# Performance work log

Measured on AMD Instinct MI355X. Metric: run time of the kernel, lower is better.

Reference implementation:

```python
import jax, jax.numpy as jnp
import numpy as np

# ---- static configuration (matches init_kwargs / input_specs) ----
B, DIM, H, W = 2, 32, 512, 512
FOLD, P, HDIM, NCLS, CV = 8, 2, 96, 16, 96
S = P * P                      # superpixels per tile
h, w = H // FOLD, W // FOLD    # 64, 64 tile size
N = h * w                      # pixels per tile

# ---- static SSN neighbor tables (init label map -> 9 candidate spixels) ----
_lab = np.repeat(np.repeat(np.arange(S).reshape(P, P), h // P, 0), w // P, 1).reshape(-1)
_sy, _sx = _lab // P, _lab % P
_dy = np.repeat(np.array([-1, 0, 1]), 3)[:, None]
_dx = np.tile(np.array([-1, 0, 1]), 3)[:, None]
_ny, _nx = _sy[None] + _dy, _sx[None] + _dx
_valid = (_ny >= 0) & (_ny < P) & (_nx >= 0) & (_nx < P)
NBR = jnp.asarray(np.where(_valid, _ny * P + _nx, 0), dtype=jnp.int32)  # [9,N]
VALID = jnp.asarray(_valid)                                             # [9,N]

def _conv1x1(x, Wk, bk):
    return jnp.einsum('oc,bchw->bohw', Wk, x) + bk[None, :, None, None]

def _tiles(t):  # 'b c (f1 h) (f2 w) -> (b f1 f2) c h w'
    Bq, C = t.shape[:2]
    return t.reshape(Bq, C, FOLD, h, FOLD, w).transpose(0, 2, 4, 1, 3, 5).reshape(Bq * FOLD * FOLD, C, h, w)

def _pool(t):  # adaptive avg pool (h,w)->(P,P); returns [b,C,S]
    b, C = t.shape[:2]
    return t.reshape(b, C, P, h // P, P, w // P).mean((3, 5)).reshape(b, C, S)

def _affinity(Fp, cen):
    # Fp [b,Ctot,N], cen [b,Ctot,S]; squared-euclid dist pixel->9 neighbor spixels,
    # sparse softmax over the 9 candidates, then scatter to dense [b,S,N] affinity.
    d = (Fp * Fp).sum(1)[:, None, :] + (cen * cen).sum(1)[:, :, None] \
        - 2.0 * jnp.einsum('bcn,bcs->bsn', Fp, cen)          # [b,S,N]
    b = Fp.shape[0]
    idx = jnp.broadcast_to(NBR[None], (b, 9, N))
    d9 = jnp.where(VALID[None], jnp.take_along_axis(d, idx, axis=1), 1e16)
    aff = jax.nn.softmax(-d9, axis=1)                        # [b,9,N]
    bi = jnp.arange(b)[:, None, None]
    ni = jnp.arange(N)[None, None, :]
    return jnp.zeros((b, S, N), Fp.dtype).at[bi, idx, ni].add(jnp.where(VALID[None], aff, 0.0))

def setup_inputs():
    k = jax.random.split(jax.random.key(0), 6)
    return {
        'x': jax.random.normal(k[0], (B, DIM, H, W), jnp.float32),
        'feat': jax.random.normal(k[1], (B, CV, H, W), jnp.float32),
        'sdf_data': jax.random.normal(k[2], (B, DIM - 1, H, W), jnp.float32),
        'Wf': 0.1 * jax.random.normal(k[3], (HDIM, DIM), jnp.float32),
        'bf': jnp.zeros((HDIM,), jnp.float32),
        'Wsdf': 0.1 * jax.random.normal(k[4], (HDIM, DIM - 1), jnp.float32),
        'bsdf': jnp.zeros((HDIM,), jnp.float32),
        'gt': jax.random.randint(k[5], (B, H, W), 0, NCLS, jnp.int32),
    }

def _cluster(x, feat, sdf_data, Wf, bf, Wsdf, bsdf):
    hsi = _conv1x1(x, Wf, bf)
    sdf = _conv1x1(sdf_data, Wsdf, bsdf)
    pf = _tiles(feat).reshape(-1, CV, N)      # per-tile pixel (value) features
    df = _tiles(hsi).reshape(-1, HDIM, N)     # deep features
    sf = _tiles(sdf).reshape(-1, HDIM, N)     # sdf features
    b = pf.shape[0]
    cen_pf = _pool(pf.reshape(b, CV, h, w))
    cen_df = _pool(df.reshape(b, HDIM, h, w))
    cen_sf = _pool(sf.reshape(b, HDIM, h, w))
    value_centers = cen_pf.transpose(0, 2, 1)                # [b,S,C]
    Fall = jnp.concatenate([pf, df, sf], 1)
    # SSN iter 0: soft affinity, update pixel-feature centroids
    A0 = _affinity(Fall, jnp.concatenate([cen_pf, cen_df, cen_sf], 1))
    cen_pf = jnp.einsum('bsn,bcn->bcs', A0, pf) / (A0.sum(-1)[:, None, :] + 1e-16)
    # SSN iter 1 (last): final dense affinity; torch computes this under no_grad
    sim = jax.lax.stop_gradient(_affinity(Fall, jnp.concatenate([cen_pf, cen_df, cen_sf], 1)))
    mask = jax.nn.one_hot(jnp.argmax(sim, 1), S, axis=1, dtype=sim.dtype)   # hard argmax mask [b,S,N]
    sim = sim * mask
    out = (jnp.einsum('bsn,bnc->bsc', sim, pf.transpose(0, 2, 1)) + value_centers) \
          / (sim.sum(-1, keepdims=True) + 1.0)
    center_feat = out.reshape(B, FOLD * FOLD * S, CV)
    mask5 = mask.reshape(B, FOLD * FOLD, S, h, w)
    return center_feat, mask5

def _gen_labels(gt, mask5):
    T = FOLD * FOLD
    coef = jnp.arange(S, dtype=mask5.dtype).reshape(1, 1, S, 1, 1)
    small = (mask5 * coef).sum(2) + jnp.arange(0, T * S, S, dtype=mask5.dtype).reshape(1, T, 1, 1)
    spix_map = small.reshape(B, FOLD, FOLD, h, w).transpose(0, 1, 3, 2, 4).reshape(B, H, W)
    gt_r = gt.reshape(B, FOLD, h, FOLD, w).transpose(0, 1, 3, 2, 4).reshape(B, T, h, w) + 1
    gt_filt = (gt_r[:, :, None].astype(mask5.dtype) * mask5).reshape(B, T, S, N).astype(jnp.int32)
    count = jax.nn.one_hot(gt_filt, NCLS + 1, dtype=jnp.float32).sum(3)   # [B,T,S,NCLS+1]
    labels = count[..., 1:].transpose(0, 3, 1, 2).reshape(B, NCLS, T * S)
    return labels, spix_map

def reference(x, feat, sdf_data, Wf, bf, Wsdf, bsdf, gt):
    center_feat, mask5 = _cluster(x, feat, sdf_data, Wf, bf, Wsdf, bsdf)
    labels, spix_map = _gen_labels(gt, jax.lax.stop_gradient(mask5))
    return center_feat, labels, spix_map
```

## Files before the change

### kernel.cpp

```cpp
#include <hip/hip_runtime.h>
#include <hip/hip_bf16.h>


#define OFF_POOLX   0
#define OFF_POOLS   16384
#define OFF_CENPF0  32256
#define OFF_UDF     81408
#define OFF_USF     97792
#define OFF_GCONST  113664
#define OFF_NORM0   114176
#define OFF_NUM1    114688
#define OFF_DEN1    163840
#define OFF_CENPF1  164352
#define OFF_NORM1   213504
#define OFF_OUTNUM  214016
#define OFF_OUTDEN  263168
#define OFF_LABELS  263680
#define OFF_G       271872
#define ZERO_BASE   OFF_NUM1
#define ZERO_LEN    157184

#define OUT_CF 0
#define OUT_LB 49152
#define OUT_SP 57344

typedef float f32x4 __attribute__((ext_vector_type(4)));
typedef short bf16x8 __attribute__((ext_vector_type(8)));
typedef unsigned short u16x4 __attribute__((ext_vector_type(4)));

__device__ __forceinline__ float bf2f(unsigned short u) {
  return __uint_as_float(((unsigned)u) << 16);
}
__device__ __forceinline__ unsigned short f2bf(float f) {
  return (unsigned short)(__float_as_uint(f) >> 16);
}

__global__ __launch_bounds__(256) void k_pool(const float* __restrict__ x,
    const float* __restrict__ feat, const float* __restrict__ sdf,
    float* __restrict__ ws) {
  int plane = blockIdx.x, f1 = blockIdx.y, tid = threadIdx.x;
  {
    int lb = blockIdx.y * gridDim.x + blockIdx.x;
    if (tid < 64) {
      int zi = lb * 64 + tid;
      if (zi < ZERO_LEN) ws[ZERO_BASE + zi] = 0.f;
    }
  }
  int b = plane / 159, ch = plane % 159;
  const float* src; int c, C, cls;
  if (ch < 32)      { src = x;    C = 32; c = ch;      cls = 0; }
  else if (ch < 63) { src = sdf;  C = 31; c = ch - 32; cls = 1; }
  else              { src = feat; C = 96; c = ch - 63; cls = 2; }
  const float* base = src + ((size_t)(b*C + c)*512 + f1*64)*512;
  int half = tid >> 7, col4 = tid & 127;
  const float* p0 = base + (size_t)half*512 + (size_t)col4*4;
  f32x4 v[16];
  float acc0 = 0.f, acc1 = 0.f;
  #pragma unroll
  for (int i = 0; i < 16; ++i)
    v[i] = *reinterpret_cast<const f32x4*>(p0 + (size_t)i*1024);
  #pragma unroll
  for (int i = 0; i < 16; ++i) { f32x4 t = v[i]; acc0 += t[0] + t[1] + t[2] + t[3]; }
  #pragma unroll
  for (int i = 0; i < 16; ++i)
    v[i] = *reinterpret_cast<const f32x4*>(p0 + (size_t)(16 + i)*1024);
  #pragma unroll
  for (int i = 0; i < 16; ++i) { f32x4 t = v[i]; acc1 += t[0] + t[1] + t[2] + t[3]; }
  acc0 += __shfl_xor(acc0, 1, 64); acc0 += __shfl_xor(acc0, 2, 64); acc0 += __shfl_xor(acc0, 4, 64);
  acc1 += __shfl_xor(acc1, 1, 64); acc1 += __shfl_xor(acc1, 2, 64); acc1 += __shfl_xor(acc1, 4, 64);
  __shared__ float part[32][2];
  int lane = tid & 63;
  if ((lane & 7) == 0) {
    int f2 = col4 >> 4, qx = (col4 >> 3) & 1;
    part[(f2*2 + qx)*2 + 0][half] = acc0;
    part[(f2*2 + qx)*2 + 1][half] = acc1;
  }
  __syncthreads();
  if (tid < 32) {
    float v2 = (part[tid][0] + part[tid][1]) * (1.f/1024.f);
    int f2 = tid >> 2, qx = (tid >> 1) & 1, qy = tid & 1;
    int tile = b*64 + f1*8 + f2, s = qy*2 + qx;
    float* dst;
    if (cls == 0)      dst = ws + OFF_POOLX  + (tile*32 + c)*4;
    else if (cls == 1) dst = ws + OFF_POOLS  + (tile*31 + c)*4;
    else               dst = ws + OFF_CENPF0 + (tile*96 + c)*4;
    dst[s] = v2;
  }
}

__global__ __launch_bounds__(384) void k_centers(const float* __restrict__ Wf,
    const float* __restrict__ bfv, const float* __restrict__ Wsdf,
    const float* __restrict__ bsdf, float* __restrict__ ws) {
  int tile = blockIdx.x, tid = threadIdx.x;
  __shared__ float px[128];
  __shared__ float ps[124];
  __shared__ float cdf[384];
  __shared__ float csf[384];
  __shared__ float redg[4], redn[4];
  if (tid < 128) px[tid] = ws[OFF_POOLX + tile*128 + tid];
  if (tid < 124) ps[tid] = ws[OFF_POOLS + tile*124 + tid];
  if (tid < 4) { redg[tid] = 0.f; redn[tid] = 0.f; }
  __syncthreads();
  int c = tid % 96, s = tid / 96;
  float bc = bfv[c];
  float a = bc;
  for (int k = 0; k < 32; ++k) a += Wf[c*32 + k] * px[k*4 + s];
  cdf[c*4 + s] = a;
  float bs = bsdf[c];
  float a2 = bs;
  for (int k = 0; k < 31; ++k) a2 += Wsdf[c*31 + k] * ps[k*4 + s];
  csf[c*4 + s] = a2;
  atomicAdd(&redg[s], 2.f*(bc*a + bs*a2) - (a*a + a2*a2));
  float cp = ws[OFF_CENPF0 + tile*384 + c*4 + s];
  atomicAdd(&redn[s], cp*cp);
  __syncthreads();
  if (tid < 128) {
    int s2 = tid >> 5, k = tid & 31;
    float u = 0.f;
    for (int c2 = 0; c2 < 96; ++c2) u += Wf[c2*32 + k] * cdf[c2*4 + s2];
    ws[OFF_UDF + tile*128 + tid] = u;
  } else if (tid < 252) {
    int t2 = tid - 128, s2 = t2 / 31, k = t2 % 31;
    float u = 0.f;
    for (int c2 = 0; c2 < 96; ++c2) u += Wsdf[c2*31 + k] * csf[c2*4 + s2];
    ws[OFF_USF + tile*124 + t2] = u;
  }
  if (tid < 4) { ws[OFF_GCONST + tile*4 + tid] = redg[tid]; ws[OFF_NORM0 + tile*4 + tid] = redn[tid]; }
}

__global__ __launch_bounds__(256) void k_pass2(const float* __restrict__ x,
    const float* __restrict__ feat, const float* __restrict__ sdf,
    float* __restrict__ ws) {
  int wg = blockIdx.x, tile = wg >> 2, seg = wg & 3, tid = threadIdx.x;
  int b = tile >> 6, tl = tile & 63, f1 = tl >> 3, f2 = tl & 7;
  __shared__ float s_cpf0[384];
  __shared__ float s_udf[128];
  __shared__ float s_usf[124];
  __shared__ float s_gc[4], s_n0[4];
  __shared__ __align__(16) unsigned short s_pfT[96][264];
  __shared__ __align__(16) unsigned short s_aT[16][264];
  __shared__ __align__(16) float s_part[2][8][260];
  for (int i = tid; i < 384; i += 256) s_cpf0[i] = ws[OFF_CENPF0 + tile*384 + i];
  if (tid < 128) s_udf[tid] = ws[OFF_UDF + tile*128 + tid];
  if (tid < 124) s_usf[tid] = ws[OFF_USF + tile*124 + tid];
  if (tid < 4) { s_gc[tid] = ws[OFF_GCONST + tile*4 + tid]; s_n0[tid] = ws[OFF_NORM0 + tile*4 + tid]; }
  for (int i = tid; i < 16*264; i += 256) (&s_aT[0][0])[i] = 0;
  __syncthreads();
  int lane = tid & 63, wave = tid >> 6;
  int mrow = lane & 15, quad = lane >> 4;
  int q4 = lane * 4;
  f32x4 zero4 = {0.f, 0.f, 0.f, 0.f};
  f32x4 accC[6] = {zero4, zero4, zero4, zero4, zero4, zero4};
  float dden[4] = {0.f, 0.f, 0.f, 0.f};
  for (int chunk = 0; chunk < 4; ++chunk) {
    int pq = seg*1024 + chunk*256 + q4;
    int goq = (f1*64 + (pq >> 6))*512 + f2*64 + (pq & 63);
    const float* xq = x   + (size_t)(b*32)*262144 + goq;
    const float* sq = sdf + (size_t)(b*31)*262144 + goq;
    const float* fq = feat+ (size_t)(b*96)*262144 + goq;
    f32x4 dpd[4] = {zero4, zero4, zero4, zero4};
    f32x4 dpp[4] = {zero4, zero4, zero4, zero4};
    f32x4 vv[8];
    #pragma unroll
    for (int i = 0; i < 8; ++i)
      vv[i] = *reinterpret_cast<const f32x4*>(xq + (size_t)(wave + 4*i)*262144);
    #pragma unroll
    for (int i = 0; i < 8; ++i) {
      int ch = wave + 4*i;
      #pragma unroll
      for (int s = 0; s < 4; ++s) dpd[s] += vv[i] * s_udf[s*32 + ch];
    }
    #pragma unroll
    for (int i = 0; i < 8; ++i)
      if (wave + 4*i < 31)
        vv[i] = *reinterpret_cast<const f32x4*>(sq + (size_t)(wave + 4*i)*262144);
    #pragma unroll
    for (int i = 0; i < 8; ++i) {
      int ch = wave + 4*i;
      if (ch < 31) {
        #pragma unroll
        for (int s = 0; s < 4; ++s) dpd[s] += vv[i] * s_usf[s*31 + ch];
      }
    }
    #pragma unroll
    for (int r = 0; r < 3; ++r) {
      #pragma unroll
      for (int i = 0; i < 8; ++i)
        vv[i] = *reinterpret_cast<const f32x4*>(fq + (size_t)(wave + 4*(r*8 + i))*262144);
      #pragma unroll
      for (int i = 0; i < 8; ++i) {
        int ch = wave + 4*(r*8 + i);
        u16x4 uu = { f2bf(vv[i][0]), f2bf(vv[i][1]), f2bf(vv[i][2]), f2bf(vv[i][3]) };
        *reinterpret_cast<u16x4*>(&s_pfT[ch][q4]) = uu;
        #pragma unroll
        for (int s = 0; s < 4; ++s) dpp[s] += vv[i] * s_cpf0[ch*4 + s];
      }
    }
    if (wave >= 2) {
      #pragma unroll
      for (int s = 0; s < 4; ++s) {
        *reinterpret_cast<f32x4*>(&s_part[wave-2][s][q4]) = dpd[s];
        *reinterpret_cast<f32x4*>(&s_part[wave-2][4+s][q4]) = dpp[s];
      }
    }
    __syncthreads();
    if (wave < 2) {
      #pragma unroll
      for (int s = 0; s < 4; ++s) {
        f32x4 t = *reinterpret_cast<f32x4*>(&s_part[wave][s][q4]);
        t += dpd[s];
        *reinterpret_cast<f32x4*>(&s_part[wave][s][q4]) = t;
        f32x4 t2 = *reinterpret_cast<f32x4*>(&s_part[wave][4+s][q4]);
        t2 += dpp[s];
        *reinterpret_cast<f32x4*>(&s_part[wave][4+s][q4]) = t2;
      }
    }
    __syncthreads();
    float d0 = s_part[0][0][tid] + s_part[1][0][tid];
    float d1 = s_part[0][1][tid] + s_part[1][1][tid];
    float d2 = s_part[0][2][tid] + s_part[1][2][tid];
    float d3 = s_part[0][3][tid] + s_part[1][3][tid];
    float p0 = s_part[0][4][tid] + s_part[1][4][tid];
    float p1 = s_part[0][5][tid] + s_part[1][5][tid];
    float p2 = s_part[0][6][tid] + s_part[1][6][tid];
    float p3 = s_part[0][7][tid] + s_part[1][7][tid];
    float g0 = 2.f*d0 + s_gc[0], g1 = 2.f*d1 + s_gc[1];
    float g2 = 2.f*d2 + s_gc[2], g3 = 2.f*d3 + s_gc[3];
    int p = seg*1024 + chunk*256 + tid;
    {
      f32x4 gv = {g0, g1, g2, g3};
      *reinterpret_cast<f32x4*>(ws + OFF_G + ((size_t)tile << 14) + (size_t)p*4) = gv;
    }
    float sc0 = g0 + 2.f*p0 - s_n0[0];
    float sc1 = g1 + 2.f*p1 - s_n0[1];
    float sc2 = g2 + 2.f*p2 - s_n0[2];
    float sc3 = g3 + 2.f*p3 - s_n0[3];
    float m = fmaxf(fmaxf(sc0, sc1), fmaxf(sc2, sc3));
    float e0 = expf(sc0 - m), e1 = expf(sc1 - m), e2 = expf(sc2 - m), e3 = expf(sc3 - m);
    float inv = 1.f / (e0 + e1 + e2 + e3);
    float a0 = e0*inv, a1 = e1*inv, a2 = e2*inv, a3 = e3*inv;
    s_aT[0][tid] = f2bf(a0); s_aT[1][tid] = f2bf(a1);
    s_aT[2][tid] = f2bf(a2); s_aT[3][tid] = f2bf(a3);
    dden[0] += a0; dden[1] += a1; dden[2] += a2; dden[3] += a3;
    __syncthreads();
    #pragma unroll
    for (int kk = 0; kk < 2; ++kk) {
      int k0 = (wave*2 + kk)*32 + quad*8;
      bf16x8 bfrag = *reinterpret_cast<const bf16x8*>(&s_aT[mrow][k0]);
      #pragma unroll
      for (int mt = 0; mt < 6; ++mt) {
        bf16x8 afrag = *reinterpret_cast<const bf16x8*>(&s_pfT[mt*16 + mrow][k0]);
        accC[mt] = __builtin_amdgcn_mfma_f32_16x16x32_bf16(afrag, bfrag, accC[mt], 0, 0, 0);
      }
    }
    __syncthreads();
  }
  if (mrow < 4) {
    #pragma unroll
    for (int mt = 0; mt < 6; ++mt)
      #pragma unroll
      for (int r = 0; r < 4; ++r) {
        int c = mt*16 + quad*4 + r;
        atomicAdd(&ws[OFF_NUM1 + (tile*96 + c)*4 + mrow], accC[mt][r]);
      }
  }
  for (int m2 = 1; m2 < 64; m2 <<= 1) {
    dden[0] += __shfl_xor(dden[0], m2, 64); dden[1] += __shfl_xor(dden[1], m2, 64);
    dden[2] += __shfl_xor(dden[2], m2, 64); dden[3] += __shfl_xor(dden[3], m2, 64);
  }
  if (lane == 0) {
    atomicAdd(&ws[OFF_DEN1 + tile*4 + 0], dden[0]);
    atomicAdd(&ws[OFF_DEN1 + tile*4 + 1], dden[1]);
    atomicAdd(&ws[OFF_DEN1 + tile*4 + 2], dden[2]);
    atomicAdd(&ws[OFF_DEN1 + tile*4 + 3], dden[3]);
  }
}

__global__ __launch_bounds__(256) void k_pass3(const float* __restrict__ feat,
    const int* __restrict__ gt, float* __restrict__ ws, float* __restrict__ out) {
  int wg = blockIdx.x, tile = wg >> 2, seg = wg & 3, tid = threadIdx.x;
  int b = tile >> 6, tl = tile & 63, f1 = tl >> 3, f2 = tl & 7;
  __shared__ float s_cpf1[384];
  __shared__ float s_n1[4];
  __shared__ __align__(16) unsigned short s_pfT[96][264];
  __shared__ __align__(16) unsigned short s_aT[16][264];
  __shared__ __align__(16) float s_part[2][4][260];
  __shared__ float s_hist[64];
  if (tid < 4) s_n1[tid] = 0.f;
  if (tid < 64) s_hist[tid] = 0.f;
  for (int i = tid; i < 16*264; i += 256) (&s_aT[0][0])[i] = 0;
  __syncthreads();
  for (int i = tid; i < 384; i += 256) {
    float den = ws[OFF_DEN1 + tile*4 + (i & 3)];
    float v = ws[OFF_NUM1 + tile*384 + i] / (den + 1e-16f);
    s_cpf1[i] = v;
    atomicAdd(&s_n1[i & 3], v*v);
  }
  __syncthreads();
  int lane = tid & 63, wave = tid >> 6;
  int mrow = lane & 15, quad = lane >> 4;
  int q4 = lane * 4;
  f32x4 zero4 = {0.f, 0.f, 0.f, 0.f};
  f32x4 accC[6] = {zero4, zero4, zero4, zero4, zero4, zero4};
  float oden[4] = {0.f, 0.f, 0.f, 0.f};
  for (int chunk = 0; chunk < 4; ++chunk) {
    int pq = seg*1024 + chunk*256 + q4;
    int goq = (f1*64 + (pq >> 6))*512 + f2*64 + (pq & 63);
    const float* fq = feat + (size_t)(b*96)*262144 + goq;
    f32x4 dpp[4] = {zero4, zero4, zero4, zero4};
    f32x4 vv[8];
    #pragma unroll
    for (int r = 0; r < 3; ++r) {
      #pragma unroll
      for (int i = 0; i < 8; ++i)
        vv[i] = *reinterpret_cast<const f32x4*>(fq + (size_t)(wave + 4*(r*8 + i))*262144);
      #pragma unroll
      for (int i = 0; i < 8; ++i) {
        int ch = wave + 4*(r*8 + i);
        u16x4 uu = { f2bf(vv[i][0]), f2bf(vv[i][1]), f2bf(vv[i][2]), f2bf(vv[i][3]) };
        *reinterpret_cast<u16x4*>(&s_pfT[ch][q4]) = uu;
        #pragma unroll
        for (int s = 0; s < 4; ++s) dpp[s] += vv[i] * s_cpf1[ch*4 + s];
      }
    }
    if (wave >= 2) {
      #pragma unroll
      for (int s = 0; s < 4; ++s)
        *reinterpret_cast<f32x4*>(&s_part[wave-2][s][q4]) = dpp[s];
    }
    __syncthreads();
    if (wave < 2) {
      #pragma unroll
      for (int s = 0; s < 4; ++s) {
        f32x4 t = *reinterpret_cast<f32x4*>(&s_part[wave][s][q4]);
        t += dpp[s];
        *reinterpret_cast<f32x4*>(&s_part[wave][s][q4]) = t;
      }
    }
    __syncthreads();
    int p = seg*1024 + chunk*256 + tid;
    int y = p >> 6, xx = p & 63;
    int go = (f1*64 + y)*512 + f2*64 + xx;
    f32x4 gv = *reinterpret_cast<const f32x4*>(ws + OFF_G + ((size_t)tile << 14) + (size_t)p*4);
    float p0 = s_part[0][0][tid] + s_part[1][0][tid];
    float p1 = s_part[0][1][tid] + s_part[1][1][tid];
    float p2 = s_part[0][2][tid] + s_part[1][2][tid];
    float p3 = s_part[0][3][tid] + s_part[1][3][tid];
    float sc0 = gv[0] + 2.f*p0 - s_n1[0];
    float sc1 = gv[1] + 2.f*p1 - s_n1[1];
    float sc2 = gv[2] + 2.f*p2 - s_n1[2];
    float sc3 = gv[3] + 2.f*p3 - s_n1[3];
    int ss = 0; float best = sc0;
    if (sc1 > best) { best = sc1; ss = 1; }
    if (sc2 > best) { best = sc2; ss = 2; }
    if (sc3 > best) { best = sc3; ss = 3; }
    float se = expf(sc0-best) + expf(sc1-best) + expf(sc2-best) + expf(sc3-best);
    float sim = 1.f / se;
    unsigned short sb = f2bf(sim);
    s_aT[0][tid] = (ss == 0) ? sb : (unsigned short)0;
    s_aT[1][tid] = (ss == 1) ? sb : (unsigned short)0;
    s_aT[2][tid] = (ss == 2) ? sb : (unsigned short)0;
    s_aT[3][tid] = (ss == 3) ? sb : (unsigned short)0;
    oden[ss] += sim;
    int gvv = gt[b*262144 + go];
    atomicAdd(&s_hist[ss*16 + gvv], 1.f);
    out[OUT_SP + b*262144 + go] = (float)(tl*4 + ss);
    __syncthreads();
    #pragma unroll
    for (int kk = 0; kk < 2; ++kk) {
      int k0 = (wave*2 + kk)*32 + quad*8;
      bf16x8 bfrag = *reinterpret_cast<const bf16x8*>(&s_aT[mrow][k0]);
      #pragma unroll
      for (int mt = 0; mt < 6; ++mt) {
        bf16x8 afrag = *reinterpret_cast<const bf16x8*>(&s_pfT[mt*16 + mrow][k0]);
        accC[mt] = __builtin_amdgcn_mfma_f32_16x16x32_bf16(afrag, bfrag, accC[mt], 0, 0, 0);
      }
    }
    __syncthreads();
  }
  if (mrow < 4) {
    #pragma unroll
    for (int mt = 0; mt < 6; ++mt)
      #pragma unroll
      for (int r = 0; r < 4; ++r) {
        int c = mt*16 + quad*4 + r;
        atomicAdd(&ws[OFF_OUTNUM + (tile*96 + c)*4 + mrow], accC[mt][r]);
      }
  }
  for (int m2 = 1; m2 < 64; m2 <<= 1) {
    oden[0] += __shfl_xor(oden[0], m2, 64); oden[1] += __shfl_xor(oden[1], m2, 64);
    oden[2] += __shfl_xor(oden[2], m2, 64); oden[3] += __shfl_xor(oden[3], m2, 64);
  }
  if (lane == 0) {
    atomicAdd(&ws[OFF_OUTDEN + tile*4 + 0], oden[0]);
    atomicAdd(&ws[OFF_OUTDEN + tile*4 + 1], oden[1]);
    atomicAdd(&ws[OFF_OUTDEN + tile*4 + 2], oden[2]);
    atomicAdd(&ws[OFF_OUTDEN + tile*4 + 3], oden[3]);
  }
  if (tid < 64) atomicAdd(&ws[OFF_LABELS + tile*64 + tid], s_hist[tid]);
}

__global__ __launch_bounds__(384) void k_out(const float* __restrict__ ws,
                                             float* __restrict__ out) {
  int tile = blockIdx.x, tid = threadIdx.x;
  int b = tile >> 6, tl = tile & 63;
  int c = tid % 96, s = tid / 96;
  float od = ws[OFF_OUTDEN + tile*4 + s];
  float v = (ws[OFF_OUTNUM + (tile*96 + c)*4 + s] + ws[OFF_CENPF0 + (tile*96 + c)*4 + s]) / (od + 1.f);
  out[OUT_CF + (size_t)(b*256 + tl*4 + s)*96 + c] = v;
  if (tid < 64) {
    int s2 = tid >> 4, cls = tid & 15;
    float cnt = ws[OFF_LABELS + tile*64 + tid];
    out[OUT_LB + (b*16 + cls)*256 + tl*4 + s2] = cnt;
  }
}

extern "C" void kernel_launch(void* const* d_in, const int* in_sizes, int n_in,
                              void* d_out, int out_size, void* d_ws, size_t ws_size,
                              hipStream_t stream) {
  const float* x    = (const float*)d_in[0];
  const float* feat = (const float*)d_in[1];
  const float* sdf  = (const float*)d_in[2];
  const float* Wf   = (const float*)d_in[3];
  const float* bfv  = (const float*)d_in[4];
  const float* Wsdf = (const float*)d_in[5];
  const float* bsdf = (const float*)d_in[6];
  const int* gt = (const int*)d_in[7];
  float* ws = (float*)d_ws;
  float* out = (float*)d_out;

  k_pool   <<<dim3(318, 8), 256, 0, stream>>>(x, feat, sdf, ws);
  k_centers<<<128, 384, 0, stream>>>(Wf, bfv, Wsdf, bsdf, ws);
  k_pass2  <<<512, 256, 0, stream>>>(x, feat, sdf, ws);
  k_pass3  <<<512, 256, 0, stream>>>(feat, gt, ws, out);
  k_out    <<<128, 384, 0, stream>>>(ws, out);
}
```

Measured before the change: 491.8 us.

## Fuse center computation into pass2 and prefetch next chunk loads in registers

Removes the k_centers launch and recomputes the per-tile center projections inside k_pass2, four times redundantly per tile, using the s_pfT buffer as scratch. Both pass kernels now software-pipeline the global loads. The next chunk's x/sdf/feat (and G/gt in pass3) go into registers while the current chunk is being computed. Launch bounds are set to 2 waves/SIMD. The register-held prefetch (~40 f32x4) raises register pressure and may spill, and the redundant center compute adds serial work before the main loop.

```diff
diff --git a/kernel.cpp b/kernel.cpp
--- a/kernel.cpp
+++ b/kernel.cpp
@@ -5,14 +5,8 @@
 #define OFF_POOLX   0
 #define OFF_POOLS   16384
 #define OFF_CENPF0  32256
-#define OFF_UDF     81408
-#define OFF_USF     97792
-#define OFF_GCONST  113664
-#define OFF_NORM0   114176
 #define OFF_NUM1    114688
 #define OFF_DEN1    163840
-#define OFF_CENPF1  164352
-#define OFF_NORM1   213504
 #define OFF_OUTNUM  214016
 #define OFF_OUTDEN  263168
 #define OFF_LABELS  263680
@@ -24,13 +18,12 @@
 #define OUT_LB 49152
 #define OUT_SP 57344
 
+#define PL 262144
+
 typedef float f32x4 __attribute__((ext_vector_type(4)));
 typedef short bf16x8 __attribute__((ext_vector_type(8)));
 typedef unsigned short u16x4 __attribute__((ext_vector_type(4)));
 
-__device__ __forceinline__ float bf2f(unsigned short u) {
-  return __uint_as_float(((unsigned)u) << 16);
-}
 __device__ __forceinline__ unsigned short f2bf(float f) {
   return (unsigned short)(__float_as_uint(f) >> 16);
 }
@@ -88,48 +81,10 @@
   }
 }
 
-__global__ __launch_bounds__(384) void k_centers(const float* __restrict__ Wf,
-    const float* __restrict__ bfv, const float* __restrict__ Wsdf,
-    const float* __restrict__ bsdf, float* __restrict__ ws) {
-  int tile = blockIdx.x, tid = threadIdx.x;
-  __shared__ float px[128];
-  __shared__ float ps[124];
-  __shared__ float cdf[384];
-  __shared__ float csf[384];
-  __shared__ float redg[4], redn[4];
-  if (tid < 128) px[tid] = ws[OFF_POOLX + tile*128 + tid];
-  if (tid < 124) ps[tid] = ws[OFF_POOLS + tile*124 + tid];
-  if (tid < 4) { redg[tid] = 0.f; redn[tid] = 0.f; }
-  __syncthreads();
-  int c = tid % 96, s = tid / 96;
-  float bc = bfv[c];
-  float a = bc;
-  for (int k = 0; k < 32; ++k) a += Wf[c*32 + k] * px[k*4 + s];
-  cdf[c*4 + s] = a;
-  float bs = bsdf[c];
-  float a2 = bs;
-  for (int k = 0; k < 31; ++k) a2 += Wsdf[c*31 + k] * ps[k*4 + s];
-  csf[c*4 + s] = a2;
-  atomicAdd(&redg[s], 2.f*(bc*a + bs*a2) - (a*a + a2*a2));
-  float cp = ws[OFF_CENPF0 + tile*384 + c*4 + s];
-  atomicAdd(&redn[s], cp*cp);
-  __syncthreads();
-  if (tid < 128) {
-    int s2 = tid >> 5, k = tid & 31;
-    float u = 0.f;
-    for (int c2 = 0; c2 < 96; ++c2) u += Wf[c2*32 + k] * cdf[c2*4 + s2];
-    ws[OFF_UDF + tile*128 + tid] = u;
-  } else if (tid < 252) {
-    int t2 = tid - 128, s2 = t2 / 31, k = t2 % 31;
-    float u = 0.f;
-    for (int c2 = 0; c2 < 96; ++c2) u += Wsdf[c2*31 + k] * csf[c2*4 + s2];
-    ws[OFF_USF + tile*124 + t2] = u;
-  }
-  if (tid < 4) { ws[OFF_GCONST + tile*4 + tid] = redg[tid]; ws[OFF_NORM0 + tile*4 + tid] = redn[tid]; }
-}
-
-__global__ __launch_bounds__(256) void k_pass2(const float* __restrict__ x,
+__global__ __launch_bounds__(256, 2) void k_pass2(const float* __restrict__ x,
     const float* __restrict__ feat, const float* __restrict__ sdf,
+    const float* __restrict__ Wf, const float* __restrict__ bfv,
+    const float* __restrict__ Wsdf, const float* __restrict__ bsdf,
     float* __restrict__ ws) {
   int wg = blockIdx.x, tile = wg >> 2, seg = wg & 3, tid = threadIdx.x;
   int b = tile >> 6, tl = tile & 63, f1 = tl >> 3, f2 = tl & 7;
@@ -140,10 +95,46 @@
   __shared__ __align__(16) unsigned short s_pfT[96][264];
   __shared__ __align__(16) unsigned short s_aT[16][264];
   __shared__ __align__(16) float s_part[2][8][260];
+  float* scr  = reinterpret_cast<float*>(&s_pfT[0][0]);
+  float* c_px = scr;
+  float* c_ps = scr + 128;
+  float* c_df = scr + 256;
+  float* c_sf = scr + 640;
   for (int i = tid; i < 384; i += 256) s_cpf0[i] = ws[OFF_CENPF0 + tile*384 + i];
-  if (tid < 128) s_udf[tid] = ws[OFF_UDF + tile*128 + tid];
-  if (tid < 124) s_usf[tid] = ws[OFF_USF + tile*124 + tid];
-  if (tid < 4) { s_gc[tid] = ws[OFF_GCONST + tile*4 + tid]; s_n0[tid] = ws[OFF_NORM0 + tile*4 + tid]; }
+  if (tid < 128) c_px[tid] = ws[OFF_POOLX + tile*128 + tid];
+  if (tid < 124) c_ps[tid] = ws[OFF_POOLS + tile*124 + tid];
+  __syncthreads();
+  for (int i = tid; i < 384; i += 256) {
+    int c = i % 96, s = i / 96;
+    float a = bfv[c];
+    for (int k = 0; k < 32; ++k) a += Wf[c*32 + k] * c_px[k*4 + s];
+    c_df[c*4 + s] = a;
+    float a2 = bsdf[c];
+    for (int k = 0; k < 31; ++k) a2 += Wsdf[c*31 + k] * c_ps[k*4 + s];
+    c_sf[c*4 + s] = a2;
+  }
+  __syncthreads();
+  if (tid < 128) {
+    int s2 = tid >> 5, k = tid & 31;
+    float u = 0.f;
+    for (int c2 = 0; c2 < 96; ++c2) u += Wf[c2*32 + k] * c_df[c2*4 + s2];
+    s_udf[tid] = u;
+  } else if (tid < 252) {
+    int t2 = tid - 128, s2 = t2 / 31, k = t2 % 31;
+    float u = 0.f;
+    for (int c2 = 0; c2 < 96; ++c2) u += Wsdf[c2*31 + k] * c_sf[c2*4 + s2];
+    s_usf[t2] = u;
+  } else {
+    int s = tid - 252;
+    float g = 0.f, n = 0.f;
+    for (int c = 0; c < 96; ++c) {
+      float a = c_df[c*4 + s], a2 = c_sf[c*4 + s];
+      g += 2.f*(bfv[c]*a + bsdf[c]*a2) - (a*a + a2*a2);
+      float cp = s_cpf0[c*4 + s];
+      n += cp*cp;
+    }
+    s_gc[s] = g; s_n0[s] = n;
+  }
   for (int i = tid; i < 16*264; i += 256) (&s_aT[0][0])[i] = 0;
   __syncthreads();
   int lane = tid & 63, wave = tid >> 6;
@@ -152,49 +143,66 @@
   f32x4 zero4 = {0.f, 0.f, 0.f, 0.f};
   f32x4 accC[6] = {zero4, zero4, zero4, zero4, zero4, zero4};
   float dden[4] = {0.f, 0.f, 0.f, 0.f};
+  const float* xb = x   + (size_t)(b*32)*PL;
+  const float* sb = sdf + (size_t)(b*31)*PL;
+  const float* fb = feat+ (size_t)(b*96)*PL;
+  f32x4 xv[8], sv[8], fv[24];
+  {
+    int pq = seg*1024 + q4;
+    int goq = (f1*64 + (pq >> 6))*512 + f2*64 + (pq & 63);
+    #pragma unroll
+    for (int i = 0; i < 8; ++i)
+      xv[i] = *reinterpret_cast<const f32x4*>(xb + (size_t)(wave + 4*i)*PL + goq);
+    #pragma unroll
+    for (int i = 0; i < 8; ++i)
+      if (wave + 4*i < 31)
+        sv[i] = *reinterpret_cast<const f32x4*>(sb + (size_t)(wave + 4*i)*PL + goq);
+    #pragma unroll
+    for (int i = 0; i < 24; ++i)
+      fv[i] = *reinterpret_cast<const f32x4*>(fb + (size_t)(wave + 4*i)*PL + goq);
+  }
   for (int chunk = 0; chunk < 4; ++chunk) {
-    int pq = seg*1024 + chunk*256 + q4;
-    int goq = (f1*64 + (pq >> 6))*512 + f2*64 + (pq & 63);
-    const float* xq = x   + (size_t)(b*32)*262144 + goq;
-    const float* sq = sdf + (size_t)(b*31)*262144 + goq;
-    const float* fq = feat+ (size_t)(b*96)*262144 + goq;
+    int pq1 = seg*1024 + (chunk+1)*256 + q4;
+    int goq1 = (f1*64 + (pq1 >> 6))*512 + f2*64 + (pq1 & 63);
     f32x4 dpd[4] = {zero4, zero4, zero4, zero4};
     f32x4 dpp[4] = {zero4, zero4, zero4, zero4};
-    f32x4 vv[8];
-    #pragma unroll
-    for (int i = 0; i < 8; ++i)
-      vv[i] = *reinterpret_cast<const f32x4*>(xq + (size_t)(wave + 4*i)*262144);
     #pragma unroll
     for (int i = 0; i < 8; ++i) {
       int ch = wave + 4*i;
       #pragma unroll
-      for (int s = 0; s < 4; ++s) dpd[s] += vv[i] * s_udf[s*32 + ch];
-    }
-    #pragma unroll
-    for (int i = 0; i < 8; ++i)
-      if (wave + 4*i < 31)
-        vv[i] = *reinterpret_cast<const f32x4*>(sq + (size_t)(wave + 4*i)*262144);
+      for (int s = 0; s < 4; ++s) dpd[s] += xv[i] * s_udf[s*32 + ch];
+    }
+    if (chunk < 3) {
+      #pragma unroll
+      for (int i = 0; i < 8; ++i)
+        xv[i] = *reinterpret_cast<const f32x4*>(xb + (size_t)(wave + 4*i)*PL + goq1);
+    }
     #pragma unroll
     for (int i = 0; i < 8; ++i) {
       int ch = wave + 4*i;
       if (ch < 31) {
         #pragma unroll
-        for (int s = 0; s < 4; ++s) dpd[s] += vv[i] * s_usf[s*31 + ch];
-      }
-    }
-    #pragma unroll
-    for (int r = 0; r < 3; ++r) {
+        for (int s = 0; s < 4; ++s) dpd[s] += sv[i] * s_usf[s*31 + ch];
+      }
+    }
+    if (chunk < 3) {
       #pragma unroll
       for (int i = 0; i < 8; ++i)
-        vv[i] = *reinterpret_cast<const f32x4*>(fq + (size_t)(wave + 4*(r*8 + i))*262144);
-      #pragma unroll
-      for (int i = 0; i < 8; ++i) {
-        int ch = wave + 4*(r*8 + i);
-        u16x4 uu = { f2bf(vv[i][0]), f2bf(vv[i][1]), f2bf(vv[i][2]), f2bf(vv[i][3]) };
-        *reinterpret_cast<u16x4*>(&s_pfT[ch][q4]) = uu;
-        #pragma unroll
-        for (int s = 0; s < 4; ++s) dpp[s] += vv[i] * s_cpf0[ch*4 + s];
-      }
+        if (wave + 4*i < 31)
+          sv[i] = *reinterpret_cast<const f32x4*>(sb + (size_t)(wave + 4*i)*PL + goq1);
+    }
+    #pragma unroll
+    for (int i = 0; i < 24; ++i) {
+      int ch = wave + 4*i;
+      u16x4 uu = { f2bf(fv[i][0]), f2bf(fv[i][1]), f2bf(fv[i][2]), f2bf(fv[i][3]) };
+      *reinterpret_cast<u16x4*>(&s_pfT[ch][q4]) = uu;
+      #pragma unroll
+      for (int s = 0; s < 4; ++s) dpp[s] += fv[i] * s_cpf0[ch*4 + s];
+    }
+    if (chunk < 3) {
+      #pragma unroll
+      for (int i = 0; i < 24; ++i)
+        fv[i] = *reinterpret_cast<const f32x4*>(fb + (size_t)(wave + 4*i)*PL + goq1);
     }
     if (wave >= 2) {
       #pragma unroll
@@ -276,7 +284,7 @@
   }
 }
 
-__global__ __launch_bounds__(256) void k_pass3(const float* __restrict__ feat,
+__global__ __launch_bounds__(256, 2) void k_pass3(const float* __restrict__ feat,
     const int* __restrict__ gt, float* __restrict__ ws, float* __restrict__ out) {
   int wg = blockIdx.x, tile = wg >> 2, seg = wg & 3, tid = threadIdx.x;
   int b = tile >> 6, tl = tile & 63, f1 = tl >> 3, f2 = tl & 7;
@@ -286,15 +294,17 @@
   __shared__ __align__(16) unsigned short s_aT[16][264];
   __shared__ __align__(16) float s_part[2][4][260];
   __shared__ float s_hist[64];
-  if (tid < 4) s_n1[tid] = 0.f;
   if (tid < 64) s_hist[tid] = 0.f;
   for (int i = tid; i < 16*264; i += 256) (&s_aT[0][0])[i] = 0;
-  __syncthreads();
   for (int i = tid; i < 384; i += 256) {
     float den = ws[OFF_DEN1 + tile*4 + (i & 3)];
-    float v = ws[OFF_NUM1 + tile*384 + i] / (den + 1e-16f);
-    s_cpf1[i] = v;
-    atomicAdd(&s_n1[i & 3], v*v);
+    s_cpf1[i] = ws[OFF_NUM1 + tile*384 + i] / (den + 1e-16f);
+  }
+  __syncthreads();
+  if (tid < 4) {
+    float n = 0.f;
+    for (int c = 0; c < 96; ++c) { float v = s_cpf1[c*4 + tid]; n += v*v; }
+    s_n1[tid] = n;
   }
   __syncthreads();
   int lane = tid & 63, wave = tid >> 6;
@@ -303,25 +313,38 @@
   f32x4 zero4 = {0.f, 0.f, 0.f, 0.f};
   f32x4 accC[6] = {zero4, zero4, zero4, zero4, zero4, zero4};
   float oden[4] = {0.f, 0.f, 0.f, 0.f};
+  const float* fb = feat + (size_t)(b*96)*PL;
+  f32x4 fv[24]; f32x4 gfut; int gtfut;
+  {
+    int pq = seg*1024 + q4;
+    int goq = (f1*64 + (pq >> 6))*512 + f2*64 + (pq & 63);
+    #pragma unroll
+    for (int i = 0; i < 24; ++i)
+      fv[i] = *reinterpret_cast<const f32x4*>(fb + (size_t)(wave + 4*i)*PL + goq);
+    int p0i = seg*1024 + tid;
+    gfut = *reinterpret_cast<const f32x4*>(ws + OFF_G + ((size_t)tile << 14) + (size_t)p0i*4);
+    gtfut = gt[b*262144 + (f1*64 + (p0i >> 6))*512 + f2*64 + (p0i & 63)];
+  }
   for (int chunk = 0; chunk < 4; ++chunk) {
-    int pq = seg*1024 + chunk*256 + q4;
-    int goq = (f1*64 + (pq >> 6))*512 + f2*64 + (pq & 63);
-    const float* fq = feat + (size_t)(b*96)*262144 + goq;
+    int pq1 = seg*1024 + (chunk+1)*256 + q4;
+    int goq1 = (f1*64 + (pq1 >> 6))*512 + f2*64 + (pq1 & 63);
     f32x4 dpp[4] = {zero4, zero4, zero4, zero4};
-    f32x4 vv[8];
-    #pragma unroll
-    for (int r = 0; r < 3; ++r) {
-      #pragma unroll
-      for (int i = 0; i < 8; ++i)
-        vv[i] = *reinterpret_cast<const f32x4*>(fq + (size_t)(wave + 4*(r*8 + i))*262144);
-      #pragma unroll
-      for (int i = 0; i < 8; ++i) {
-        int ch = wave + 4*(r*8 + i);
-        u16x4 uu = { f2bf(vv[i][0]), f2bf(vv[i][1]), f2bf(vv[i][2]), f2bf(vv[i][3]) };
-        *reinterpret_cast<u16x4*>(&s_pfT[ch][q4]) = uu;
-        #pragma unroll
-        for (int s = 0; s < 4; ++s) dpp[s] += vv[i] * s_cpf1[ch*4 + s];
-      }
+    f32x4 gcur = gfut; int gtcur = gtfut;
+    #pragma unroll
+    for (int i = 0; i < 24; ++i) {
+      int ch = wave + 4*i;
+      u16x4 uu = { f2bf(fv[i][0]), f2bf(fv[i][1]), f2bf(fv[i][2]), f2bf(fv[i][3]) };
+      *reinterpret_cast<u16x4*>(&s_pfT[ch][q4]) = uu;
+      #pragma unroll
+      for (int s = 0; s < 4; ++s) dpp[s] += fv[i] * s_cpf1[ch*4 + s];
+    }
+    if (chunk < 3) {
+      #pragma unroll
+      for (int i = 0; i < 24; ++i)
+        fv[i] = *reinterpret_cast<const f32x4*>(fb + (size_t)(wave + 4*i)*PL + goq1);
+      int p1i = seg*1024 + (chunk+1)*256 + tid;
+      gfut = *reinterpret_cast<const f32x4*>(ws + OFF_G + ((size_t)tile << 14) + (size_t)p1i*4);
+      gtfut = gt[b*262144 + (f1*64 + (p1i >> 6))*512 + f2*64 + (p1i & 63)];
     }
     if (wave >= 2) {
       #pragma unroll
@@ -339,17 +362,15 @@
     }
     __syncthreads();
     int p = seg*1024 + chunk*256 + tid;
-    int y = p >> 6, xx = p & 63;
-    int go = (f1*64 + y)*512 + f2*64 + xx;
-    f32x4 gv = *reinterpret_cast<const f32x4*>(ws + OFF_G + ((size_t)tile << 14) + (size_t)p*4);
+    int go = (f1*64 + (p >> 6))*512 + f2*64 + (p & 63);
     float p0 = s_part[0][0][tid] + s_part[1][0][tid];
     float p1 = s_part[0][1][tid] + s_part[1][1][tid];
     float p2 = s_part[0][2][tid] + s_part[1][2][tid];
     float p3 = s_part[0][3][tid] + s_part[1][3][tid];
-    float sc0 = gv[0] + 2.f*p0 - s_n1[0];
-    float sc1 = gv[1] + 2.f*p1 - s_n1[1];
-    float sc2 = gv[2] + 2.f*p2 - s_n1[2];
-    float sc3 = gv[3] + 2.f*p3 - s_n1[3];
+    float sc0 = gcur[0] + 2.f*p0 - s_n1[0];
+    float sc1 = gcur[1] + 2.f*p1 - s_n1[1];
+    float sc2 = gcur[2] + 2.f*p2 - s_n1[2];
+    float sc3 = gcur[3] + 2.f*p3 - s_n1[3];
     int ss = 0; float best = sc0;
     if (sc1 > best) { best = sc1; ss = 1; }
     if (sc2 > best) { best = sc2; ss = 2; }
@@ -362,8 +383,7 @@
     s_aT[2][tid] = (ss == 2) ? sb : (unsigned short)0;
     s_aT[3][tid] = (ss == 3) ? sb : (unsigned short)0;
     oden[ss] += sim;
-    int gvv = gt[b*262144 + go];
-    atomicAdd(&s_hist[ss*16 + gvv], 1.f);
+    atomicAdd(&s_hist[ss*16 + gtcur], 1.f);
     out[OUT_SP + b*262144 + go] = (float)(tl*4 + ss);
     __syncthreads();
     #pragma unroll
@@ -429,9 +449,8 @@
   float* ws = (float*)d_ws;
   float* out = (float*)d_out;
 
-  k_pool   <<<dim3(318, 8), 256, 0, stream>>>(x, feat, sdf, ws);
-  k_centers<<<128, 384, 0, stream>>>(Wf, bfv, Wsdf, bsdf, ws);
-  k_pass2  <<<512, 256, 0, stream>>>(x, feat, sdf, ws);
-  k_pass3  <<<512, 256, 0, stream>>>(feat, gt, ws, out);
-  k_out    <<<128, 384, 0, stream>>>(ws, out);
-}
+  k_pool <<<dim3(318, 8), 256, 0, stream>>>(x, feat, sdf, ws);
+  k_pass2<<<512, 256, 0, stream>>>(x, feat, sdf, Wf, bfv, Wsdf, bsdf, ws);
+  k_pass3<<<512, 256, 0, stream>>>(feat, gt, ws, out);
+  k_out  <<<128, 384, 0, stream>>>(ws, out);
+}
```

New measurement: 812.2 us. 1.65x slower.
